# Kernel tuning notes

Measured on AMD Instinct MI355X. Metric: run time of the kernel, lower is better.

Reference implementation:

```python
import jax, jax.numpy as jnp
import numpy as np

EMBED_DIM = 1024
NUM_HEADS = 16
HEAD_DIM = EMBED_DIM // NUM_HEADS


def setup_inputs() -> dict:
    key = jax.random.key(0)
    k1, k2, k3, k4, k5 = jax.random.split(key, 5)
    B, L, C = 4, 4096, EMBED_DIM
    s = 1.0 / np.sqrt(C)
    return {
        "x": jax.random.normal(k1, (B, L, C), dtype=jnp.float32),
        "qkv_w": jax.random.normal(k2, (3 * C, C), dtype=jnp.float32) * s,
        "qkv_b": jax.random.normal(k3, (3 * C,), dtype=jnp.float32) * 0.01,
        "out_w": jax.random.normal(k4, (C, C), dtype=jnp.float32) * s,
        "out_b": jax.random.normal(k5, (C,), dtype=jnp.float32) * 0.01,
        "num_frames": 16,
    }


def reference(x, qkv_w, qkv_b, out_w, out_b, num_frames):
    B, L, C = x.shape
    P = L // num_frames  # patches per frame
    H, D = NUM_HEADS, HEAD_DIM
    xf = x.reshape(B * num_frames, P, C)
    # fused QKV projection (torch Linear: y = x @ W^T + b)
    qkv = xf @ qkv_w.T + qkv_b                      # [BF, P, 3C]
    qkv = qkv.reshape(B * num_frames, P, 3, H, D)
    qkv = jnp.transpose(qkv, (2, 0, 3, 1, 4))        # [3, BF, H, P, D]
    q, k, v = qkv[0], qkv[1], qkv[2]
    scores = jnp.einsum("bhqd,bhkd->bhqk", q, k) / np.sqrt(D)
    attn = jax.nn.softmax(scores, axis=-1)
    out = jnp.einsum("bhqk,bhkd->bhqd", attn, v)     # [BF, H, P, D]
    out = jnp.transpose(out, (0, 2, 1, 3)).reshape(B, L, C)
    return out @ out_w.T + out_b
```

## Files before the change

kernel.cpp:

```cpp
#include <hip/hip_runtime.h>


typedef __bf16 bf16x8 __attribute__((ext_vector_type(8)));
typedef float f32x4 __attribute__((ext_vector_type(4)));

__device__ __forceinline__ void gload_lds16(const void* g, void* l) {
  __builtin_amdgcn_global_load_lds(
      (__attribute__((address_space(1))) void*)(g),
      (__attribute__((address_space(3))) void*)(l), 16, 0, 0);
}

__global__ __launch_bounds__(256) void cvt_f32_bf16(
    const float* __restrict__ in, __bf16* __restrict__ out, int n8) {
  int i = blockIdx.x * 256 + threadIdx.x;
  if (i >= n8) return;
  const float4* p = (const float4*)in;
  float4 a = p[2 * i];
  float4 b = p[2 * i + 1];
  bf16x8 v;
  v[0] = (__bf16)a.x; v[1] = (__bf16)a.y; v[2] = (__bf16)a.z; v[3] = (__bf16)a.w;
  v[4] = (__bf16)b.x; v[5] = (__bf16)b.y; v[6] = (__bf16)b.z; v[7] = (__bf16)b.w;
  ((bf16x8*)out)[i] = v;
}

template <bool BF16_OUT>
__global__ __launch_bounds__(512, 2) void gemm256(
    const __bf16* __restrict__ A, const __bf16* __restrict__ Bm,
    const float* __restrict__ bias, void* __restrict__ Cv,
    int M, int N, int K) {
  __shared__ alignas(16) __bf16 Al[2][256 * 64];
  __shared__ alignas(16) __bf16 Bl[2][256 * 64];

  const int tid = threadIdx.x, lane = tid & 63, wid = tid >> 6;
  const int wr = wid >> 2, wc = wid & 3;
  const int l15 = lane & 15, l4 = lane >> 4;

  const int nwg = gridDim.x * gridDim.y;
  const int bid = blockIdx.y * gridDim.x + blockIdx.x;
  const int q = nwg >> 3;
  const int swz = (bid & 7) * q + (bid >> 3);
  const int bn = swz % gridDim.x, bm = swz / gridDim.x;

  const int NT = K >> 6;

  const __bf16* gA[4];
  const __bf16* gB[4];
#pragma unroll
  for (int c = 0; c < 4; ++c) {
    int seg = c * 512 + tid;
    int row = seg >> 3, bl = (seg & 7) ^ (row & 7);
    gA[c] = A + (size_t)(bm * 256 + row) * K + bl * 8;
    gB[c] = Bm + (size_t)(bn * 256 + row) * K + bl * 8;
  }

#define STAGE(b)                                         \
  {                                                      \
    _Pragma("unroll") for (int c = 0; c < 4; ++c) {      \
      gload_lds16(gA[c], &Al[b][(c * 512 + tid) * 8]);   \
      gA[c] += 64;                                       \
    }                                                    \
    _Pragma("unroll") for (int c = 0; c < 4; ++c) {      \
      gload_lds16(gB[c], &Bl[b][(c * 512 + tid) * 8]);   \
      gB[c] += 64;                                       \
    }                                                    \
  }

  const int rsw = l15 & 7;
  const int pk0 = ((l4) ^ rsw) * 8;
  const int pk1 = ((4 + l4) ^ rsw) * 8;
  const int aRow = (wr * 128 + l15) * 64;
  const int bRow = (wc * 64 + l15) * 64;

  f32x4 acc[8][4] = {};

  STAGE(0);
  STAGE(1);
  asm volatile("s_waitcnt vmcnt(8)" ::: "memory");
  __builtin_amdgcn_s_barrier();

  for (int t = 0; t < NT; ++t) {
    const __bf16* Ab = &Al[t & 1][0];
    const __bf16* Bb = &Bl[t & 1][0];
    const bool hasStage = (t + 2 < NT);
    const bool hasNext = (t + 1 < NT);

    bf16x8 b0 = *(const bf16x8*)(Bb + bRow + 0 * 1024 + pk0);
    bf16x8 b1 = *(const bf16x8*)(Bb + bRow + 1 * 1024 + pk0);
    bf16x8 b2 = *(const bf16x8*)(Bb + bRow + 2 * 1024 + pk0);
    bf16x8 b3 = *(const bf16x8*)(Bb + bRow + 3 * 1024 + pk0);
    bf16x8 x0 = *(const bf16x8*)(Ab + aRow + 0 * 1024 + pk0);
    bf16x8 x1 = *(const bf16x8*)(Ab + aRow + 1 * 1024 + pk0);
    bf16x8 x2 = *(const bf16x8*)(Ab + aRow + 2 * 1024 + pk0);
    bf16x8 x3 = *(const bf16x8*)(Ab + aRow + 3 * 1024 + pk0);
    __builtin_amdgcn_s_setprio(1);
#pragma unroll
    for (int n = 0; n < 4; ++n) {
      bf16x8 bb = n == 0 ? b0 : n == 1 ? b1 : n == 2 ? b2 : b3;
      acc[0][n] = __builtin_amdgcn_mfma_f32_16x16x32_bf16(x0, bb, acc[0][n], 0, 0, 0);
      acc[1][n] = __builtin_amdgcn_mfma_f32_16x16x32_bf16(x1, bb, acc[1][n], 0, 0, 0);
      acc[2][n] = __builtin_amdgcn_mfma_f32_16x16x32_bf16(x2, bb, acc[2][n], 0, 0, 0);
      acc[3][n] = __builtin_amdgcn_mfma_f32_16x16x32_bf16(x3, bb, acc[3][n], 0, 0, 0);
    }
    __builtin_amdgcn_s_setprio(0);

    x0 = *(const bf16x8*)(Ab + aRow + 4 * 1024 + pk0);
    x1 = *(const bf16x8*)(Ab + aRow + 5 * 1024 + pk0);
    x2 = *(const bf16x8*)(Ab + aRow + 6 * 1024 + pk0);
    x3 = *(const bf16x8*)(Ab + aRow + 7 * 1024 + pk0);
    __builtin_amdgcn_s_setprio(1);
#pragma unroll
    for (int n = 0; n < 4; ++n) {
      bf16x8 bb = n == 0 ? b0 : n == 1 ? b1 : n == 2 ? b2 : b3;
      acc[4][n] = __builtin_amdgcn_mfma_f32_16x16x32_bf16(x0, bb, acc[4][n], 0, 0, 0);
      acc[5][n] = __builtin_amdgcn_mfma_f32_16x16x32_bf16(x1, bb, acc[5][n], 0, 0, 0);
      acc[6][n] = __builtin_amdgcn_mfma_f32_16x16x32_bf16(x2, bb, acc[6][n], 0, 0, 0);
      acc[7][n] = __builtin_amdgcn_mfma_f32_16x16x32_bf16(x3, bb, acc[7][n], 0, 0, 0);
    }
    __builtin_amdgcn_s_setprio(0);

    b0 = *(const bf16x8*)(Bb + bRow + 0 * 1024 + pk1);
    b1 = *(const bf16x8*)(Bb + bRow + 1 * 1024 + pk1);
    b2 = *(const bf16x8*)(Bb + bRow + 2 * 1024 + pk1);
    b3 = *(const bf16x8*)(Bb + bRow + 3 * 1024 + pk1);
    x0 = *(const bf16x8*)(Ab + aRow + 0 * 1024 + pk1);
    x1 = *(const bf16x8*)(Ab + aRow + 1 * 1024 + pk1);
    x2 = *(const bf16x8*)(Ab + aRow + 2 * 1024 + pk1);
    x3 = *(const bf16x8*)(Ab + aRow + 3 * 1024 + pk1);
    __builtin_amdgcn_s_setprio(1);
#pragma unroll
    for (int n = 0; n < 4; ++n) {
      bf16x8 bb = n == 0 ? b0 : n == 1 ? b1 : n == 2 ? b2 : b3;
      acc[0][n] = __builtin_amdgcn_mfma_f32_16x16x32_bf16(x0, bb, acc[0][n], 0, 0, 0);
      acc[1][n] = __builtin_amdgcn_mfma_f32_16x16x32_bf16(x1, bb, acc[1][n], 0, 0, 0);
      acc[2][n] = __builtin_amdgcn_mfma_f32_16x16x32_bf16(x2, bb, acc[2][n], 0, 0, 0);
      acc[3][n] = __builtin_amdgcn_mfma_f32_16x16x32_bf16(x3, bb, acc[3][n], 0, 0, 0);
    }
    __builtin_amdgcn_s_setprio(0);

    x0 = *(const bf16x8*)(Ab + aRow + 4 * 1024 + pk1);
    x1 = *(const bf16x8*)(Ab + aRow + 5 * 1024 + pk1);
    x2 = *(const bf16x8*)(Ab + aRow + 6 * 1024 + pk1);
    x3 = *(const bf16x8*)(Ab + aRow + 7 * 1024 + pk1);
    asm volatile("s_waitcnt lgkmcnt(0)" ::: "memory");
    __builtin_amdgcn_sched_barrier(0);
    __builtin_amdgcn_s_barrier();
    if (hasStage) STAGE(t & 1);
    __builtin_amdgcn_s_setprio(1);
#pragma unroll
    for (int n = 0; n < 4; ++n) {
      bf16x8 bb = n == 0 ? b0 : n == 1 ? b1 : n == 2 ? b2 : b3;
      acc[4][n] = __builtin_amdgcn_mfma_f32_16x16x32_bf16(x0, bb, acc[4][n], 0, 0, 0);
      acc[5][n] = __builtin_amdgcn_mfma_f32_16x16x32_bf16(x1, bb, acc[5][n], 0, 0, 0);
      acc[6][n] = __builtin_amdgcn_mfma_f32_16x16x32_bf16(x2, bb, acc[6][n], 0, 0, 0);
      acc[7][n] = __builtin_amdgcn_mfma_f32_16x16x32_bf16(x3, bb, acc[7][n], 0, 0, 0);
    }
    __builtin_amdgcn_s_setprio(0);
    if (hasNext) {
      if (hasStage)
        asm volatile("s_waitcnt vmcnt(8)" ::: "memory");
      else
        asm volatile("s_waitcnt vmcnt(0)" ::: "memory");
      __builtin_amdgcn_s_barrier();
    }
  }
#undef STAGE

  const int r0 = l4 * 4;
#pragma unroll
  for (int m = 0; m < 8; ++m) {
#pragma unroll
    for (int n = 0; n < 4; ++n) {
      int row = bm * 256 + wr * 128 + m * 16 + r0;
      int col = bn * 256 + wc * 64 + n * 16 + l15;
      float bb = bias[col];
#pragma unroll
      for (int r = 0; r < 4; ++r) {
        float v = acc[m][n][r] + bb;
        if (BF16_OUT)
          ((__bf16*)Cv)[(size_t)(row + r) * N + col] = (__bf16)v;
        else
          ((float*)Cv)[(size_t)(row + r) * N + col] = v;
      }
    }
  }
}

__global__ __launch_bounds__(256, 2) void attn_kernel(
    const __bf16* __restrict__ qkv, __bf16* __restrict__ attnOut) {
  __shared__ alignas(16) __bf16 Ks[256 * 64];
  __shared__ alignas(16) __bf16 Vt[64 * 256];
  __shared__ alignas(16) __bf16 Pl[4][64 * 32];

  const int h = blockIdx.x, bf = blockIdx.y;
  const int tid = threadIdx.x, lane = tid & 63, wid = tid >> 6;
  const int l15 = lane & 15, l4 = lane >> 4;

  const __bf16* base = qkv + (size_t)(bf * 256) * 3072 + h * 64;

#pragma unroll
  for (int rr = 0; rr < 8; ++rr) {
    int s = rr * 256 + wid * 64 + lane;
    int r = s >> 3, t = s & 7, c8 = t ^ (r & 7);
    gload_lds16(base + 1024 + (size_t)r * 3072 + c8 * 8, &Ks[s * 8]);
  }

  {
    const __bf16* vrow = base + 2048 + (size_t)tid * 3072;
    bf16x8 vv[8];
#pragma unroll
    for (int b8 = 0; b8 < 8; ++b8) vv[b8] = *(const bf16x8*)(vrow + b8 * 8);
#pragma unroll
    for (int b8 = 0; b8 < 8; ++b8)
#pragma unroll
      for (int e = 0; e < 8; ++e) {
        int d = b8 * 8 + e;
        Vt[d * 256 + (((tid >> 3) ^ (d & 7)) * 8) + (tid & 7)] = vv[b8][e];
      }
  }

  bf16x8 aq[4][2];
  const __bf16* qbase = base + (size_t)(wid * 64) * 3072;
#pragma unroll
  for (int m = 0; m < 4; ++m)
#pragma unroll
    for (int kk = 0; kk < 2; ++kk)
      aq[m][kk] =
          *(const bf16x8*)(qbase + (size_t)(m * 16 + l15) * 3072 + kk * 32 + l4 * 8);

  __syncthreads();

  float m_run[4][4], lsum[4][4];
#pragma unroll
  for (int m = 0; m < 4; ++m)
#pragma unroll
    for (int r = 0; r < 4; ++r) { m_run[m][r] = -3.0e38f; lsum[m][r] = 0.f; }
  f32x4 o[4][4] = {};

  __bf16* Pw = &Pl[wid][0];

  for (int jt = 0; jt < 4; ++jt) {
    f32x4 s[4][4] = {};
#pragma unroll
    for (int kk = 0; kk < 2; ++kk) {
      bf16x8 bk[4];
#pragma unroll
      for (int n = 0; n < 4; ++n) {
        int j = jt * 64 + n * 16 + l15;
        int c8 = kk * 4 + l4;
        bk[n] = *(const bf16x8*)&Ks[(j * 8 + (c8 ^ (j & 7))) * 8];
      }
      __builtin_amdgcn_s_setprio(1);
#pragma unroll
      for (int m = 0; m < 4; ++m)
#pragma unroll
        for (int n = 0; n < 4; ++n)
          s[m][n] = __builtin_amdgcn_mfma_f32_16x16x32_bf16(aq[m][kk], bk[n],
                                                            s[m][n], 0, 0, 0);
      __builtin_amdgcn_s_setprio(0);
    }
#pragma unroll
    for (int m = 0; m < 4; ++m)
#pragma unroll
      for (int n = 0; n < 4; ++n) s[m][n] *= 0.125f;
    float tloc[4][4];
    float grow = 0.f;
#pragma unroll
    for (int m = 0; m < 4; ++m)
#pragma unroll
      for (int r = 0; r < 4; ++r) {
        float t = fmaxf(fmaxf(s[m][0][r], s[m][1][r]),
                        fmaxf(s[m][2][r], s[m][3][r]));
        t = fmaxf(t, __shfl_xor(t, 1));
        t = fmaxf(t, __shfl_xor(t, 2));
        t = fmaxf(t, __shfl_xor(t, 4));
        t = fmaxf(t, __shfl_xor(t, 8));
        tloc[m][r] = t;
        grow = fmaxf(grow, t - m_run[m][r]);
      }
    if (__any(grow > 8.0f)) {
#pragma unroll
      for (int m = 0; m < 4; ++m)
#pragma unroll
        for (int r = 0; r < 4; ++r) {
          float mn = fmaxf(m_run[m][r], tloc[m][r]);
          float al = __expf(m_run[m][r] - mn);
          m_run[m][r] = mn;
          lsum[m][r] *= al;
#pragma unroll
          for (int nd = 0; nd < 4; ++nd) o[m][nd][r] *= al;
        }
    }
#pragma unroll
    for (int m = 0; m < 4; ++m)
#pragma unroll
      for (int r = 0; r < 4; ++r) {
        float p0 = __expf(s[m][0][r] - m_run[m][r]);
        float p1 = __expf(s[m][1][r] - m_run[m][r]);
        float p2 = __expf(s[m][2][r] - m_run[m][r]);
        float p3 = __expf(s[m][3][r] - m_run[m][r]);
        s[m][0][r] = p0; s[m][1][r] = p1; s[m][2][r] = p2; s[m][3][r] = p3;
        lsum[m][r] += (p0 + p1) + (p2 + p3);
      }
#pragma unroll
    for (int hh = 0; hh < 2; ++hh) {
#pragma unroll
      for (int m = 0; m < 4; ++m)
#pragma unroll
        for (int nn = 0; nn < 2; ++nn)
#pragma unroll
          for (int r = 0; r < 4; ++r) {
            int qr = m * 16 + l4 * 4 + r;
            int j = nn * 16 + l15;
            Pw[qr * 32 + (((j >> 3) ^ (qr & 3)) * 8) + (j & 7)] =
                (__bf16)s[m][2 * hh + nn][r];
          }
      bf16x8 ap[4];
#pragma unroll
      for (int m = 0; m < 4; ++m) {
        int qr = m * 16 + l15;
        ap[m] = *(const bf16x8*)&Pw[qr * 32 + ((l4 ^ (qr & 3)) * 8)];
      }
      bf16x8 bv[4];
#pragma unroll
      for (int nd = 0; nd < 4; ++nd) {
        int d = nd * 16 + l15;
        int jb = jt * 8 + hh * 4 + l4;
        bv[nd] = *(const bf16x8*)&Vt[d * 256 + ((jb ^ (d & 7)) * 8)];
      }
      __builtin_amdgcn_s_setprio(1);
#pragma unroll
      for (int m = 0; m < 4; ++m)
#pragma unroll
        for (int nd = 0; nd < 4; ++nd)
          o[m][nd] = __builtin_amdgcn_mfma_f32_16x16x32_bf16(ap[m], bv[nd],
                                                             o[m][nd], 0, 0, 0);
      __builtin_amdgcn_s_setprio(0);
    }
  }

  __bf16* ob = attnOut + (size_t)(bf * 256 + wid * 64) * 1024 + h * 64;
#pragma unroll
  for (int m = 0; m < 4; ++m)
#pragma unroll
    for (int r = 0; r < 4; ++r) {
      float rs = lsum[m][r];
      rs += __shfl_xor(rs, 1);
      rs += __shfl_xor(rs, 2);
      rs += __shfl_xor(rs, 4);
      rs += __shfl_xor(rs, 8);
      float inv = 1.0f / rs;
#pragma unroll
      for (int nd = 0; nd < 4; ++nd)
        ob[(size_t)(m * 16 + l4 * 4 + r) * 1024 + nd * 16 + l15] =
            (__bf16)(o[m][nd][r] * inv);
    }
}

extern "C" void kernel_launch(void* const* d_in, const int* in_sizes, int n_in,
                              void* d_out, int out_size, void* d_ws,
                              size_t ws_size, hipStream_t stream) {
  const float* x = (const float*)d_in[0];
  const float* qkv_w = (const float*)d_in[1];
  const float* qkv_b = (const float*)d_in[2];
  const float* out_w = (const float*)d_in[3];
  const float* out_b = (const float*)d_in[4];
  float* out = (float*)d_out;

  __bf16* xb = (__bf16*)d_ws;
  __bf16* qkvwb = xb + 16777216;
  __bf16* outwb = qkvwb + 3145728;
  __bf16* qkvb = outwb + 1048576;
  __bf16* attnb = qkvb + (size_t)16384 * 3072;

  cvt_f32_bf16<<<8192, 256, 0, stream>>>(x, xb, 16777216 / 8);
  cvt_f32_bf16<<<1536, 256, 0, stream>>>(qkv_w, qkvwb, 3145728 / 8);
  cvt_f32_bf16<<<512, 256, 0, stream>>>(out_w, outwb, 1048576 / 8);

  gemm256<true><<<dim3(12, 64), 512, 0, stream>>>(xb, qkvwb, qkv_b, qkvb,
                                                  16384, 3072, 1024);

  attn_kernel<<<dim3(16, 64), 256, 0, stream>>>(qkvb, attnb);

  gemm256<false><<<dim3(4, 64), 512, 0, stream>>>(attnb, outwb, out_b, out,
                                                  16384, 1024, 1024);
}
```

Before: 358.6 us.

## Write QKV as per-head contiguous panels and stage attention output through LDS

The QKV GEMM epilogue now scatters its output into separate Q, K and V buffers laid out per (frame, head) as contiguous 256x64 panels, instead of a row-major [tokens, 3072] matrix. The attention kernel reads these panels with contiguous 128-byte rows, avoiding strided 3072-element row accesses when loading K, V and Q. The attention epilogue also stages normalized outputs in the per-wave LDS scratch so it can issue 16-byte vector stores instead of scalar bf16 stores. The cost is a more scattered GEMM epilogue store pattern and some extra LDS traffic at the end of attention.

```diff
diff --git a/kernel.cpp b/kernel.cpp
--- a/kernel.cpp
+++ b/kernel.cpp
@@ -23,7 +23,7 @@
   ((bf16x8*)out)[i] = v;
 }
 
-template <bool BF16_OUT>
+template <int MODE>
 __global__ __launch_bounds__(512, 2) void gemm256(
     const __bf16* __restrict__ A, const __bf16* __restrict__ Bm,
     const float* __restrict__ bias, void* __restrict__ Cv,
@@ -166,27 +166,41 @@
 #undef STAGE
 
   const int r0 = l4 * 4;
-#pragma unroll
-  for (int m = 0; m < 8; ++m) {
-#pragma unroll
-    for (int n = 0; n < 4; ++n) {
-      int row = bm * 256 + wr * 128 + m * 16 + r0;
-      int col = bn * 256 + wc * 64 + n * 16 + l15;
-      float bb = bias[col];
-#pragma unroll
-      for (int r = 0; r < 4; ++r) {
-        float v = acc[m][n][r] + bb;
-        if (BF16_OUT)
-          ((__bf16*)Cv)[(size_t)(row + r) * N + col] = (__bf16)v;
-        else
-          ((float*)Cv)[(size_t)(row + r) * N + col] = v;
+  if (MODE == 1) {
+    const int sel = bn >> 2;
+    const int hh = (bn * 4 + wc) & 15;
+    __bf16* pan = (__bf16*)Cv + (size_t)sel * 16777216 +
+                  (size_t)(bm * 16 + hh) * 16384;
+#pragma unroll
+    for (int m = 0; m < 8; ++m) {
+#pragma unroll
+      for (int n = 0; n < 4; ++n) {
+        int p = wr * 128 + m * 16 + r0;
+        int d = n * 16 + l15;
+        float bb = bias[bn * 256 + wc * 64 + n * 16 + l15];
+#pragma unroll
+        for (int r = 0; r < 4; ++r)
+          pan[(size_t)(p + r) * 64 + d] = (__bf16)(acc[m][n][r] + bb);
+      }
+    }
+  } else {
+#pragma unroll
+    for (int m = 0; m < 8; ++m) {
+#pragma unroll
+      for (int n = 0; n < 4; ++n) {
+        int row = bm * 256 + wr * 128 + m * 16 + r0;
+        int col = bn * 256 + wc * 64 + n * 16 + l15;
+        float bb = bias[col];
+#pragma unroll
+        for (int r = 0; r < 4; ++r)
+          ((float*)Cv)[(size_t)(row + r) * N + col] = acc[m][n][r] + bb;
       }
     }
   }
 }
 
 __global__ __launch_bounds__(256, 2) void attn_kernel(
-    const __bf16* __restrict__ qkv, __bf16* __restrict__ attnOut) {
+    const __bf16* __restrict__ qkv3, __bf16* __restrict__ attnOut) {
   __shared__ alignas(16) __bf16 Ks[256 * 64];
   __shared__ alignas(16) __bf16 Vt[64 * 256];
   __shared__ alignas(16) __bf16 Pl[4][64 * 32];
@@ -195,17 +209,20 @@
   const int tid = threadIdx.x, lane = tid & 63, wid = tid >> 6;
   const int l15 = lane & 15, l4 = lane >> 4;
 
-  const __bf16* base = qkv + (size_t)(bf * 256) * 3072 + h * 64;
+  const size_t g = (size_t)(bf * 16 + h) * 16384;
+  const __bf16* Qp = qkv3 + g;
+  const __bf16* Kp = qkv3 + 16777216 + g;
+  const __bf16* Vp = qkv3 + 33554432 + g;
 
 #pragma unroll
   for (int rr = 0; rr < 8; ++rr) {
-    int s = rr * 256 + wid * 64 + lane;
+    int s = rr * 256 + tid;
     int r = s >> 3, t = s & 7, c8 = t ^ (r & 7);
-    gload_lds16(base + 1024 + (size_t)r * 3072 + c8 * 8, &Ks[s * 8]);
+    gload_lds16(Kp + r * 64 + c8 * 8, &Ks[s * 8]);
   }
 
   {
-    const __bf16* vrow = base + 2048 + (size_t)tid * 3072;
+    const __bf16* vrow = Vp + (size_t)tid * 64;
     bf16x8 vv[8];
 #pragma unroll
     for (int b8 = 0; b8 < 8; ++b8) vv[b8] = *(const bf16x8*)(vrow + b8 * 8);
@@ -219,13 +236,12 @@
   }
 
   bf16x8 aq[4][2];
-  const __bf16* qbase = base + (size_t)(wid * 64) * 3072;
 #pragma unroll
   for (int m = 0; m < 4; ++m)
 #pragma unroll
     for (int kk = 0; kk < 2; ++kk)
-      aq[m][kk] =
-          *(const bf16x8*)(qbase + (size_t)(m * 16 + l15) * 3072 + kk * 32 + l4 * 8);
+      aq[m][kk] = *(const bf16x8*)(Qp + (size_t)(wid * 64 + m * 16 + l15) * 64 +
+                                   kk * 32 + l4 * 8);
 
   __syncthreads();
 
@@ -338,7 +354,7 @@
     }
   }
 
-  __bf16* ob = attnOut + (size_t)(bf * 256 + wid * 64) * 1024 + h * 64;
+  float inv[4][4];
 #pragma unroll
   for (int m = 0; m < 4; ++m)
 #pragma unroll
@@ -348,12 +364,29 @@
       rs += __shfl_xor(rs, 2);
       rs += __shfl_xor(rs, 4);
       rs += __shfl_xor(rs, 8);
-      float inv = 1.0f / rs;
-#pragma unroll
-      for (int nd = 0; nd < 4; ++nd)
-        ob[(size_t)(m * 16 + l4 * 4 + r) * 1024 + nd * 16 + l15] =
-            (__bf16)(o[m][nd][r] * inv);
-    }
+      inv[m][r] = 1.0f / rs;
+    }
+
+  __bf16* ob = attnOut + (size_t)(bf * 256 + wid * 64) * 1024 + h * 64;
+#pragma unroll
+  for (int c = 0; c < 2; ++c) {
+#pragma unroll
+    for (int m = 0; m < 4; ++m)
+#pragma unroll
+      for (int nn = 0; nn < 2; ++nn) {
+        int nd = c * 2 + nn;
+#pragma unroll
+        for (int r = 0; r < 4; ++r)
+          Pw[(m * 16 + l4 * 4 + r) * 32 + nn * 16 + l15] =
+              (__bf16)(o[m][nd][r] * inv[m][r]);
+      }
+#pragma unroll
+    for (int i = 0; i < 4; ++i) {
+      int rr = i * 16 + (lane >> 2);
+      bf16x8 v = *(const bf16x8*)&Pw[rr * 32 + (lane & 3) * 8];
+      *(bf16x8*)(ob + (size_t)rr * 1024 + c * 32 + (lane & 3) * 8) = v;
+    }
+  }
 }
 
 extern "C" void kernel_launch(void* const* d_in, const int* in_sizes, int n_in,
@@ -376,11 +409,11 @@
   cvt_f32_bf16<<<1536, 256, 0, stream>>>(qkv_w, qkvwb, 3145728 / 8);
   cvt_f32_bf16<<<512, 256, 0, stream>>>(out_w, outwb, 1048576 / 8);
 
-  gemm256<true><<<dim3(12, 64), 512, 0, stream>>>(xb, qkvwb, qkv_b, qkvb,
-                                                  16384, 3072, 1024);
+  gemm256<1><<<dim3(12, 64), 512, 0, stream>>>(xb, qkvwb, qkv_b, qkvb,
+                                               16384, 3072, 1024);
 
   attn_kernel<<<dim3(16, 64), 256, 0, stream>>>(qkvb, attnb);
 
-  gemm256<false><<<dim3(4, 64), 512, 0, stream>>>(attnb, outwb, out_b, out,
-                                                  16384, 1024, 1024);
+  gemm256<0><<<dim3(4, 64), 512, 0, stream>>>(attnb, outwb, out_b, out,
+                                              16384, 1024, 1024);
 }
```

Result: faster. 339.5 us (-5.3%).
